# Optimization experiments

Hardware: AMD Instinct MI355X
Metric: run time of the kernel (lower is better)

## Reference

```python
import jax, jax.numpy as jnp
import numpy as np


def setup_inputs() -> dict:
    key = jax.random.key(0)
    ks = jax.random.split(key, 9)
    B, T, C = 4, 2048, 2048
    E, I, SI = 8, 1408, 5632
    s = lambda k, shape, fan_in: jax.random.normal(k, shape, jnp.float32) * (fan_in ** -0.5)
    return {
        "x": jax.random.normal(ks[0], (B, T, C), jnp.float32),
        "gate_w": s(ks[1], (C, E), C),                  # router: x @ gate_w -> [N,E]
        "expert_gate_w": s(ks[2], (E, C, I), C),        # stacked gate_proj weights
        "expert_up_w": s(ks[3], (E, C, I), C),          # stacked up_proj weights
        "expert_down_w": s(ks[4], (E, I, C), I),        # stacked down_proj weights
        "shared_gate_w": s(ks[5], (C, SI), C),
        "shared_up_w": s(ks[6], (C, SI), C),
        "shared_down_w": s(ks[7], (SI, C), SI),
        "shared_expert_gate_w": s(ks[8], (C, 1), C),
        "top_k": 4,
    }


def reference(x, gate_w, expert_gate_w, expert_up_w, expert_down_w,
              shared_gate_w, shared_up_w, shared_down_w, shared_expert_gate_w, top_k):
    B, T, C = x.shape
    E = gate_w.shape[1]
    xf = x.reshape(-1, C)                      # [N, C]
    N = xf.shape[0]

    # --- router: softmax (fp32) -> top-k -> renormalize ---
    logits = xf @ gate_w                       # [N, E]
    probs = jax.nn.softmax(logits.astype(jnp.float32), axis=-1)
    w, idx = jax.lax.top_k(probs, top_k)       # [N, k]
    w = w / jnp.sum(w, axis=-1, keepdims=True)

    # dense combine gates [N, E]: zero for non-selected experts (equivalent to
    # the torch dispatch/sort/combine: each token gets weight w_k on expert idx_k)
    gates = jnp.zeros((N, E), jnp.float32).at[jnp.arange(N)[:, None], idx].add(w)

    # --- per-expert SwiGLU MLP, accumulated via scan over experts ---
    def step(acc, ew):
        wg, wu, wd, g = ew                     # wg/wu: [C,I], wd: [I,C], g: [N]
        h = jax.nn.silu(xf @ wg) * (xf @ wu)   # [N, I]
        return acc + g[:, None] * (h @ wd), None

    routed, _ = jax.lax.scan(
        step, jnp.zeros_like(xf),
        (expert_gate_w, expert_up_w, expert_down_w, gates.T))

    # --- shared expert with sigmoid gate ---
    shared = (jax.nn.silu(xf @ shared_gate_w) * (xf @ shared_up_w)) @ shared_down_w
    sg = jax.nn.sigmoid(xf @ shared_expert_gate_w)   # [N, 1]

    return (routed + sg * shared).reshape(B, T, C)
```

## Files before the change

### kernel.cpp

```cpp
#include <hip/hip_runtime.h>
#include <hip/hip_bf16.h>
#include <stdint.h>


typedef float f32x4 __attribute__((ext_vector_type(4)));
typedef int   i32x4 __attribute__((ext_vector_type(4)));
typedef __hip_bfloat16 bf16;

#define DEV __device__ __forceinline__

DEV void mfma16(f32x4& c, const i32x4& a, const i32x4& b) {
    asm("v_mfma_f32_16x16x32_bf16 %0, %1, %2, %0" : "+v"(c) : "v"(a), "v"(b));
}

template<int ROWS>
DEV void stage(const bf16* gtile, long ldK, char* lds, int tid) {
    const int wid = tid >> 6, lane = tid & 63;
    const int swz = ((lane & 7) ^ (lane >> 3)) << 4;
    constexpr int NISS = (ROWS * 128) / 4096;
    #pragma unroll
    for (int i = 0; i < NISS; i++) {
        const int o = i * 4096 + wid * 1024;
        const int row = (o >> 7) + (lane >> 3);
        const char* ga = (const char*)gtile + (long)row * (ldK * 2) + swz;
        __builtin_amdgcn_global_load_lds(
            (const __attribute__((address_space(1))) void*)ga,
            (__attribute__((address_space(3))) void*)(lds + o), 16, 0, 0);
    }
}

template<int ROWS>
DEV void stage_idx(const char* base, const long* roff, int ktb, char* lds,
                   int tid, int swz) {
    const int wid = tid >> 6;
    constexpr int NISS = (ROWS * 128) / 4096;
    #pragma unroll
    for (int i = 0; i < NISS; i++) {
        const int o = i * 4096 + wid * 1024;
        const char* ga = base + roff[i] + ktb + swz;
        __builtin_amdgcn_global_load_lds(
            (const __attribute__((address_space(1))) void*)ga,
            (__attribute__((address_space(3))) void*)(lds + o), 16, 0, 0);
    }
}

DEV i32x4 ldsfrag(const char* lds, int row, int kbyte) {
    const int off = (row << 7) + (kbyte ^ ((row & 7) << 4));
    return *(const i32x4*)(lds + off);
}

__global__ __launch_bounds__(256) void tcvt(const float* __restrict__ srcA,
        bf16* __restrict__ dstA, const float* __restrict__ srcB,
        bf16* __restrict__ dstB, int Cd, long dld, long sz, long dz,
        int zsplit) {
    __shared__ float t[64][65];
    long z = blockIdx.z;
    const float* src; bf16* dst;
    if ((int)z < zsplit) { src = srcA; dst = dstA; }
    else { src = srcB; dst = dstB; z -= zsplit; }
    src += z * sz; dst += z * dz;
    const int cb = blockIdx.x * 64, rb = blockIdx.y * 64;
    const int tx = threadIdx.x & 63, ty = threadIdx.x >> 6;
    #pragma unroll
    for (int i = 0; i < 16; i++) {
        const int r = ty + i * 4;
        t[r][tx] = src[(long)(rb + r) * Cd + cb + tx];
    }
    __syncthreads();
    #pragma unroll
    for (int i = 0; i < 16; i++) {
        const int c = ty + i * 4;
        dst[(long)(cb + c) * dld + rb + tx] = __float2bfloat16(t[tx][c]);
    }
}

__global__ __launch_bounds__(256) void cvtrt(const float* __restrict__ x,
        const float* __restrict__ gw, const float* __restrict__ segw,
        bf16* __restrict__ xb, int* __restrict__ tidx, float* __restrict__ tw,
        float* __restrict__ sg) {
    const int lane = threadIdx.x & 63;
    const long t = (long)blockIdx.x * 4 + (threadIdx.x >> 6);
    const float4* xr = (const float4*)(x + t * 2048);
    ushort4* xo = (ushort4*)(xb + t * 2048);
    float a[9];
    #pragma unroll
    for (int e = 0; e < 9; e++) a[e] = 0.f;
    #pragma unroll
    for (int i = 0; i < 8; i++) {
        const int c4 = i * 64 + lane;
        const float4 v = xr[c4];
        union { bf16 h[4]; ushort4 u; } cu;
        cu.h[0] = __float2bfloat16(v.x); cu.h[1] = __float2bfloat16(v.y);
        cu.h[2] = __float2bfloat16(v.z); cu.h[3] = __float2bfloat16(v.w);
        xo[c4] = cu.u;
        const int c = c4 * 4;
        const float xv[4] = { v.x, v.y, v.z, v.w };
        #pragma unroll
        for (int j = 0; j < 4; j++) {
            const float4* g4 = (const float4*)(gw + (long)(c + j) * 8);
            const float4 g0 = g4[0], g1 = g4[1];
            a[0] += xv[j] * g0.x; a[1] += xv[j] * g0.y;
            a[2] += xv[j] * g0.z; a[3] += xv[j] * g0.w;
            a[4] += xv[j] * g1.x; a[5] += xv[j] * g1.y;
            a[6] += xv[j] * g1.z; a[7] += xv[j] * g1.w;
            a[8] += xv[j] * segw[c + j];
        }
    }
    #pragma unroll
    for (int e = 0; e < 9; e++) {
        #pragma unroll
        for (int o = 32; o; o >>= 1) a[e] += __shfl_xor(a[e], o, 64);
    }
    if (lane == 0) {
        float m = a[0];
        #pragma unroll
        for (int e = 1; e < 8; e++) m = fmaxf(m, a[e]);
        float p[8]; float s = 0.f;
        #pragma unroll
        for (int e = 0; e < 8; e++) { p[e] = expf(a[e] - m); s += p[e]; }
        #pragma unroll
        for (int e = 0; e < 8; e++) p[e] /= s;
        bool used[8] = {false,false,false,false,false,false,false,false};
        float wsum = 0.f; int idx[4]; float wv[4];
        for (int k = 0; k < 4; k++) {
            float best = -1.f; int bi = 0;
            for (int e = 0; e < 8; e++)
                if (!used[e] && p[e] > best) { best = p[e]; bi = e; }
            used[bi] = true; idx[k] = bi; wv[k] = best; wsum += best;
        }
        int4 iv; float4 wv4;
        iv.x = idx[0]; iv.y = idx[1]; iv.z = idx[2]; iv.w = idx[3];
        wv4.x = wv[0] / wsum; wv4.y = wv[1] / wsum;
        wv4.z = wv[2] / wsum; wv4.w = wv[3] / wsum;
        ((int4*)tidx)[t] = iv;
        ((float4*)tw)[t] = wv4;
        sg[t] = 1.f / (1.f + expf(-a[8]));
    }
}

__global__ __launch_bounds__(256) void build_lists(const int* __restrict__ tidx,
        const float* __restrict__ tw, int* __restrict__ tok,
        float* __restrict__ wl, int* __restrict__ cnt, int N) {
    const int e = blockIdx.x;
    const int tid = threadIdx.x;
    const int per = N / 256;
    __shared__ int csum[256];
    int c = 0;
    for (int i = 0; i < per; i++) {
        const int4 id4 = ((const int4*)tidx)[tid * per + i];
        if (id4.x == e || id4.y == e || id4.z == e || id4.w == e) c++;
    }
    csum[tid] = c;
    __syncthreads();
    for (int o = 1; o < 256; o <<= 1) {
        const int v = (tid >= o) ? csum[tid - o] : 0;
        __syncthreads();
        csum[tid] += v;
        __syncthreads();
    }
    int pos = csum[tid] - c;
    if (tid == 255) cnt[e] = csum[255];
    for (int i = 0; i < per; i++) {
        const int t = tid * per + i;
        const int4   id4 = ((const int4*)tidx)[t];
        const float4 w4  = ((const float4*)tw)[t];
        float w = 0.f; int hit = 0;
        if      (id4.x == e) { w = w4.x; hit = 1; }
        else if (id4.y == e) { w = w4.y; hit = 1; }
        else if (id4.z == e) { w = w4.z; hit = 1; }
        else if (id4.w == e) { w = w4.w; hit = 1; }
        if (hit) { tok[(long)e * N + pos] = t; wl[(long)e * N + pos] = w; pos++; }
    }
}

__global__ void scan8(const int* __restrict__ cnt, int* __restrict__ starts) {
    if (threadIdx.x == 0) {
        int s = 0;
        for (int e = 0; e < 8; e++) { starts[e] = s; s += cnt[e]; }
        starts[8] = s;
    }
}

__global__ __launch_bounds__(256) void megadual(const bf16* __restrict__ A0,
        const int* __restrict__ tok, const int* __restrict__ cnt,
        const int* __restrict__ starts, int nExpZ, int e0,
        const bf16* __restrict__ Wea, const bf16* __restrict__ Web, long ebz,
        const bf16* __restrict__ Wsa, const bf16* __restrict__ Wsb,
        bf16* __restrict__ He, bf16* __restrict__ Hs,
        const float* __restrict__ wl, const float* __restrict__ sg, int K) {
    __shared__ __align__(128) char Al[16384];
    __shared__ __align__(128) char Gl[8192];
    __shared__ __align__(128) char Ul[8192];
    const int z = blockIdx.z;
    const bf16 *BG, *BU; bf16* H; long hld, n0; const float* sc;
    const int* ridx; int Me;
    if (z < nExpZ) {
        const int e = e0 + z;
        Me = cnt[e];
        ridx = tok + (long)e * 8192;
        BG = Wea + (long)z * ebz; BU = Web + (long)z * ebz;
        H = He + ((long)starts[e] - starts[e0]) * 1408;
        hld = 1408; sc = wl + (long)e * 8192;
        n0 = (long)blockIdx.y * 64;
    } else {
        Me = 8192; ridx = nullptr;
        BG = Wsa; BU = Wsb; H = Hs; hld = 5632; sc = sg;
        n0 = (long)((z - nExpZ) * gridDim.y + blockIdx.y) * 64;
    }
    const long m0 = (long)blockIdx.x * 128;
    if (m0 >= Me) return;
    const int tid = threadIdx.x, lane = tid & 63, wid = tid >> 6;
    const int wm = (wid >> 1) * 64, wn = (wid & 1) * 32;
    const int l15 = lane & 15, lhi = lane >> 4;
    const int swz = ((lane & 7) ^ (lane >> 3)) << 4;
    long roffA[4];
    #pragma unroll
    for (int i = 0; i < 4; i++) {
        const int rit = ((i * 4096 + wid * 1024) >> 7) + (lane >> 3);
        int g = (int)m0 + rit;
        if (ridx) g = ridx[g < Me ? g : Me - 1];
        roffA[i] = (long)g * (K * 2);
    }
    f32x4 ag[4][2] = {}; f32x4 au[4][2] = {};
    for (int kt = 0; kt < K; kt += 64) {
        stage_idx<128>((const char*)A0, roffA, kt * 2, Al, tid, swz);
        stage<64>(BG + n0 * K + kt, (long)K, Gl, tid);
        stage<64>(BU + n0 * K + kt, (long)K, Ul, tid);
        __syncthreads();
        #pragma unroll
        for (int ks = 0; ks < 2; ks++) {
            const int kb = ks * 64 + lhi * 16;
            i32x4 af[4], bg[2], bu[2];
            #pragma unroll
            for (int mi = 0; mi < 4; mi++) af[mi] = ldsfrag(Al, wm + mi * 16 + l15, kb);
            #pragma unroll
            for (int ni = 0; ni < 2; ni++) {
                bg[ni] = ldsfrag(Gl, wn + ni * 16 + l15, kb);
                bu[ni] = ldsfrag(Ul, wn + ni * 16 + l15, kb);
            }
            #pragma unroll
            for (int mi = 0; mi < 4; mi++) {
                #pragma unroll
                for (int ni = 0; ni < 2; ni++) {
                    mfma16(ag[mi][ni], af[mi], bg[ni]);
                    mfma16(au[mi][ni], af[mi], bu[ni]);
                }
            }
        }
        __syncthreads();
    }
    asm volatile("s_nop 7\n\ts_nop 7\n\ts_nop 7");
    #pragma unroll
    for (int mi = 0; mi < 4; mi++) {
        #pragma unroll
        for (int r = 0; r < 4; r++) {
            const int pos = (int)m0 + wm + mi * 16 + lhi * 4 + r;
            if (pos < Me) {
                const float s = sc[pos];
                #pragma unroll
                for (int ni = 0; ni < 2; ni++) {
                    const float gv = ag[mi][ni][r], uv = au[mi][ni][r];
                    const float h = (gv / (1.f + expf(-gv))) * uv * s;
                    H[(long)pos * hld + n0 + wn + ni * 16 + l15] = __float2bfloat16(h);
                }
            }
        }
    }
}

template<int TAG>
__global__ __launch_bounds__(256) void gemm_down_t(const bf16* __restrict__ A,
        const bf16* __restrict__ BT, float* __restrict__ C,
        const int* __restrict__ ridx, const int* __restrict__ cntp, int Mfix,
        const int* __restrict__ starts, int ia, int ib,
        int K, long ldc, int beta) {
    __shared__ __align__(128) char Al[16384];
    __shared__ __align__(128) char Bl[16384];
    const int Me = cntp ? *cntp : Mfix;
    const long m0 = (long)blockIdx.y * 128;
    if (m0 >= Me) return;
    if (starts) A += ((long)starts[ia] - starts[ib]) * K;
    const int tid = threadIdx.x, lane = tid & 63, wid = tid >> 6;
    const long n0 = (long)blockIdx.x * 128;
    const int wm = (wid >> 1) * 64, wn = (wid & 1) * 64;
    const int l15 = lane & 15, lhi = lane >> 4;
    f32x4 acc[4][4] = {};
    for (int kt = 0; kt < K; kt += 64) {
        stage<128>(A  + m0 * K + kt, (long)K, Al, tid);
        stage<128>(BT + n0 * K + kt, (long)K, Bl, tid);
        __syncthreads();
        #pragma unroll
        for (int ks = 0; ks < 2; ks++) {
            const int kb = ks * 64 + lhi * 16;
            i32x4 af[4], bfr[4];
            #pragma unroll
            for (int mi = 0; mi < 4; mi++) af[mi]  = ldsfrag(Al, wm + mi * 16 + l15, kb);
            #pragma unroll
            for (int ni = 0; ni < 4; ni++) bfr[ni] = ldsfrag(Bl, wn + ni * 16 + l15, kb);
            #pragma unroll
            for (int mi = 0; mi < 4; mi++) {
                #pragma unroll
                for (int ni = 0; ni < 4; ni++) mfma16(acc[mi][ni], af[mi], bfr[ni]);
            }
        }
        __syncthreads();
    }
    asm volatile("s_nop 7\n\ts_nop 7\n\ts_nop 7");
    #pragma unroll
    for (int mi = 0; mi < 4; mi++) {
        #pragma unroll
        for (int r = 0; r < 4; r++) {
            const int pos = (int)m0 + wm + mi * 16 + lhi * 4 + r;
            if (pos < Me) {
                const long orow = ridx ? (long)ridx[pos] : (long)pos;
                #pragma unroll
                for (int ni = 0; ni < 4; ni++) {
                    const long ci = orow * ldc + n0 + wn + ni * 16 + l15;
                    float v = acc[mi][ni][r];
                    if (beta) v += C[ci];
                    C[ci] = v;
                }
            }
        }
    }
}

extern "C" void kernel_launch(void* const* d_in, const int* in_sizes, int n_in,
                              void* d_out, int out_size, void* d_ws, size_t ws_size,
                              hipStream_t stream) {
    const int N = 8192, Cdim = 2048, E = 8, I = 1408, SI = 5632;

    const float* x    = (const float*)d_in[0];
    const float* gw   = (const float*)d_in[1];
    const float* egw  = (const float*)d_in[2];
    const float* euw  = (const float*)d_in[3];
    const float* edw  = (const float*)d_in[4];
    const float* sgw  = (const float*)d_in[5];
    const float* suw  = (const float*)d_in[6];
    const float* sdw  = (const float*)d_in[7];
    const float* segw = (const float*)d_in[8];
    float* out = (float*)d_out;

    char* ws = (char*)d_ws;
    size_t off = 0;
    auto alloc = [&](size_t bytes) { char* p = ws + off; off += (bytes + 255) & ~(size_t)255; return p; };

    bf16*  xb     = (bf16*) alloc((size_t)N * Cdim * 2);
    int*   tidx   = (int*)  alloc((size_t)N * 4 * 4);
    float* tw     = (float*)alloc((size_t)N * 4 * 4);
    float* sg     = (float*)alloc((size_t)N * 4);
    int*   tok    = (int*)  alloc((size_t)E * N * 4);
    float* wl     = (float*)alloc((size_t)E * N * 4);
    int*   cnt    = (int*)  alloc(256);
    int*   starts = (int*)  alloc(256);
    const size_t commonEnd = off;

    const size_t EWSLOT = (size_t)E * I * Cdim * 2;
    const size_t SWSLOT = (size_t)SI * Cdim * 2;
    const size_t HROWS  = (size_t)4 * N;
    const size_t mergedNeed = commonEnd + 2 * EWSLOT + 2 * SWSLOT
                            + (size_t)N * SI * 2 + HROWS * I * 2 + 4096;

    cvtrt<<<N / 4, 256, 0, stream>>>(x, gw, segw, xb, tidx, tw, sg);
    build_lists<<<E, 256, 0, stream>>>(tidx, tw, tok, wl, cnt, N);
    scan8<<<1, 64, 0, stream>>>(cnt, starts);

    if (ws_size >= mergedNeed) {
        bf16* Wea = (bf16*)alloc(EWSLOT);
        bf16* Web = (bf16*)alloc(EWSLOT);
        bf16* Wsa = (bf16*)alloc(SWSLOT);
        bf16* Wsb = (bf16*)alloc(SWSLOT);
        bf16* Hs  = (bf16*)alloc((size_t)N * SI * 2);
        bf16* He  = (bf16*)alloc(HROWS * I * 2);
        bf16* Wsc = Wea;
        bf16* Wec = Web;

        tcvt<<<dim3(SI / 64, Cdim / 64, 2), 256, 0, stream>>>(
                sgw, Wsa, suw, Wsb, SI, (long)Cdim, 0, 0, 1);
        tcvt<<<dim3(I / 64, Cdim / 64, 2 * E), 256, 0, stream>>>(
                egw, Wea, euw, Web, I, (long)Cdim,
                (long)Cdim * I, (long)I * Cdim, E);

        megadual<<<dim3(N / 128, I / 64, E + 4), 256, 0, stream>>>(xb,
                tok, cnt, starts, E, 0, Wea, Web, (long)I * Cdim,
                Wsa, Wsb, He, Hs, wl, sg, Cdim);

        tcvt<<<dim3(Cdim / 64, SI / 64, 1), 256, 0, stream>>>(
                sdw, Wsc, nullptr, nullptr, Cdim, (long)SI, 0, 0, 1);
        tcvt<<<dim3(Cdim / 64, I / 64, E), 256, 0, stream>>>(
                edw, Wec, nullptr, nullptr, Cdim, (long)I,
                (long)I * Cdim, (long)Cdim * I, E);

        gemm_down_t<0><<<dim3(Cdim / 128, N / 128), 256, 0, stream>>>(
                Hs, Wsc, out, nullptr, nullptr, N, nullptr, 0, 0,
                SI, (long)Cdim, 0);
        for (int e = 0; e < E; e++) {
            gemm_down_t<1><<<dim3(Cdim / 128, N / 128), 256, 0, stream>>>(
                    He, Wec + (long)e * Cdim * I, out,
                    tok + (long)e * N, cnt + e, 0, starts, e, 0,
                    I, (long)Cdim, 1);
        }
        return;
    }

    bf16* Wa = (bf16*)alloc(SWSLOT);
    bf16* Wb = (bf16*)alloc(SWSLOT);
    bf16* Wc = (bf16*)alloc(SWSLOT);
    bf16* Hs = (bf16*)alloc((size_t)N * SI * 2);
    bf16* He = (bf16*)alloc(HROWS * I * 2);
    if (off > ws_size) return;

    tcvt<<<dim3(SI / 64, Cdim / 64, 2), 256, 0, stream>>>(
            sgw, Wa, suw, Wb, SI, (long)Cdim, 0, 0, 1);
    tcvt<<<dim3(Cdim / 64, SI / 64, 1), 256, 0, stream>>>(
            sdw, Wc, nullptr, nullptr, Cdim, (long)SI, 0, 0, 1);
    megadual<<<dim3(N / 128, I / 64, 4), 256, 0, stream>>>(xb,
            tok, cnt, starts, 0, 0, nullptr, nullptr, 0,
            Wa, Wb, nullptr, Hs, wl, sg, Cdim);
    gemm_down_t<0><<<dim3(Cdim / 128, N / 128), 256, 0, stream>>>(
            Hs, Wc, out, nullptr, nullptr, N, nullptr, 0, 0, SI, (long)Cdim, 0);

    for (int b = 0; b < 2; b++) {
        const int e0 = b * 4;
        tcvt<<<dim3(I / 64, Cdim / 64, 8), 256, 0, stream>>>(
                egw + (long)e0 * Cdim * I, Wa, euw + (long)e0 * Cdim * I, Wb,
                I, (long)Cdim, (long)Cdim * I, (long)I * Cdim, 4);
        megadual<<<dim3(N / 128, I / 64, 4), 256, 0, stream>>>(xb,
                tok, cnt, starts, 4, e0, Wa, Wb, (long)I * Cdim,
                nullptr, nullptr, He, nullptr, wl, sg, Cdim);
        tcvt<<<dim3(Cdim / 64, I / 64, 4), 256, 0, stream>>>(
                edw + (long)e0 * I * Cdim, Wc, nullptr, nullptr,
                Cdim, (long)I, (long)I * Cdim, (long)Cdim * I, 4);
        for (int z = 0; z < 4; z++) {
            gemm_down_t<1><<<dim3(Cdim / 128, N / 128), 256, 0, stream>>>(
                    He, Wc + (long)z * Cdim * I, out,
                    tok + (long)(e0 + z) * N, cnt + e0 + z, 0,
                    starts, e0 + z, e0, I, (long)Cdim, 1);
        }
    }
}
```

Measured before the change: 1.576 ms.

## Batch expert down-projections into one grouped GEMM and reduce per token

The eight per-expert down-projection launches, each doing a read-modify-write scatter into the fp32 output, are replaced by a single grouped GEMM over all experts. It writes bf16 per-slot results into a contiguous buffer, and a reduce kernel sums each token's four slots into the output. build_lists now records an inverse map from token and k to list position. Workspace regions for the converted down weights and intermediates are reused. This trades fewer launches and less serialized fp32 traffic for an extra bf16 intermediate round-trip and some bf16 rounding of the expert outputs. The combine weight is still not applied in the down GEMM, so it is presumably folded into He earlier.

```diff
diff --git a/kernel.cpp b/kernel.cpp
--- a/kernel.cpp
+++ b/kernel.cpp
@@ -140,7 +140,8 @@
 
 __global__ __launch_bounds__(256) void build_lists(const int* __restrict__ tidx,
         const float* __restrict__ tw, int* __restrict__ tok,
-        float* __restrict__ wl, int* __restrict__ cnt, int N) {
+        float* __restrict__ wl, int* __restrict__ cnt, int* __restrict__ inv,
+        int N) {
     const int e = blockIdx.x;
     const int tid = threadIdx.x;
     const int per = N / 256;
@@ -164,12 +165,17 @@
         const int t = tid * per + i;
         const int4   id4 = ((const int4*)tidx)[t];
         const float4 w4  = ((const float4*)tw)[t];
-        float w = 0.f; int hit = 0;
-        if      (id4.x == e) { w = w4.x; hit = 1; }
-        else if (id4.y == e) { w = w4.y; hit = 1; }
-        else if (id4.z == e) { w = w4.z; hit = 1; }
-        else if (id4.w == e) { w = w4.w; hit = 1; }
-        if (hit) { tok[(long)e * N + pos] = t; wl[(long)e * N + pos] = w; pos++; }
+        float w = 0.f; int hit = 0; int k = 0;
+        if      (id4.x == e) { w = w4.x; hit = 1; k = 0; }
+        else if (id4.y == e) { w = w4.y; hit = 1; k = 1; }
+        else if (id4.z == e) { w = w4.z; hit = 1; k = 2; }
+        else if (id4.w == e) { w = w4.w; hit = 1; k = 3; }
+        if (hit) {
+            tok[(long)e * N + pos] = t;
+            wl[(long)e * N + pos] = w;
+            inv[t * 4 + k] = pos;
+            pos++;
+        }
     }
 }
 
@@ -325,6 +331,90 @@
     }
 }
 
+__global__ __launch_bounds__(256) void megadown(const bf16* __restrict__ He,
+        const bf16* __restrict__ Wd0, long wz, bf16* __restrict__ De,
+        const int* __restrict__ cnt, const int* __restrict__ starts, int K) {
+    __shared__ __align__(128) char Al[16384];
+    __shared__ __align__(128) char Bl[16384];
+    const int z = blockIdx.z;
+    const int Me = cnt[z];
+    const long m0 = (long)blockIdx.y * 128;
+    if (m0 >= Me) return;
+    const bf16* A  = He + (long)starts[z] * K;
+    const bf16* BT = Wd0 + (long)z * wz;
+    const int tid = threadIdx.x, lane = tid & 63, wid = tid >> 6;
+    const long n0 = (long)blockIdx.x * 128;
+    const int wm = (wid >> 1) * 64, wn = (wid & 1) * 64;
+    const int l15 = lane & 15, lhi = lane >> 4;
+    f32x4 acc[4][4] = {};
+    for (int kt = 0; kt < K; kt += 64) {
+        stage<128>(A  + m0 * K + kt, (long)K, Al, tid);
+        stage<128>(BT + n0 * K + kt, (long)K, Bl, tid);
+        __syncthreads();
+        #pragma unroll
+        for (int ks = 0; ks < 2; ks++) {
+            const int kb = ks * 64 + lhi * 16;
+            i32x4 af[4], bfr[4];
+            #pragma unroll
+            for (int mi = 0; mi < 4; mi++) af[mi]  = ldsfrag(Al, wm + mi * 16 + l15, kb);
+            #pragma unroll
+            for (int ni = 0; ni < 4; ni++) bfr[ni] = ldsfrag(Bl, wn + ni * 16 + l15, kb);
+            #pragma unroll
+            for (int mi = 0; mi < 4; mi++) {
+                #pragma unroll
+                for (int ni = 0; ni < 4; ni++) mfma16(acc[mi][ni], af[mi], bfr[ni]);
+            }
+        }
+        __syncthreads();
+    }
+    asm volatile("s_nop 7\n\ts_nop 7\n\ts_nop 7");
+    #pragma unroll
+    for (int mi = 0; mi < 4; mi++) {
+        #pragma unroll
+        for (int r = 0; r < 4; r++) {
+            const int pos = (int)m0 + wm + mi * 16 + lhi * 4 + r;
+            if (pos < Me) {
+                const long orow = (long)starts[z] + pos;
+                #pragma unroll
+                for (int ni = 0; ni < 4; ni++) {
+                    De[orow * 2048 + n0 + wn + ni * 16 + l15]
+                        = __float2bfloat16(acc[mi][ni][r]);
+                }
+            }
+        }
+    }
+}
+
+__global__ __launch_bounds__(256) void reduce4(const bf16* __restrict__ De,
+        const int* __restrict__ tidx, const int* __restrict__ inv,
+        const int* __restrict__ starts, float* __restrict__ out) {
+    const long t = blockIdx.x;
+    const int c = threadIdx.x * 8;
+    const int4 e4 = ((const int4*)tidx)[t];
+    const int4 p4 = ((const int4*)inv)[t];
+    long r[4];
+    r[0] = (long)starts[e4.x] + p4.x; r[1] = (long)starts[e4.y] + p4.y;
+    r[2] = (long)starts[e4.z] + p4.z; r[3] = (long)starts[e4.w] + p4.w;
+    float4* o = (float4*)(out + t * 2048 + c);
+    float4 o0 = o[0], o1 = o[1];
+    float acc[8] = { o0.x, o0.y, o0.z, o0.w, o1.x, o1.y, o1.z, o1.w };
+    #pragma unroll
+    for (int k = 0; k < 4; k++) {
+        const uint4 v = *(const uint4*)(De + r[k] * 2048 + c);
+        const unsigned w[4] = { v.x, v.y, v.z, v.w };
+        #pragma unroll
+        for (int j = 0; j < 4; j++) {
+            union { unsigned u; float f; } lo, hi;
+            lo.u = (w[j] & 0xffffu) << 16;
+            hi.u = w[j] & 0xffff0000u;
+            acc[j * 2]     += lo.f;
+            acc[j * 2 + 1] += hi.f;
+        }
+    }
+    o[0] = make_float4(acc[0], acc[1], acc[2], acc[3]);
+    o[1] = make_float4(acc[4], acc[5], acc[6], acc[7]);
+}
+
 extern "C" void kernel_launch(void* const* d_in, const int* in_sizes, int n_in,
                               void* d_out, int out_size, void* d_ws, size_t ws_size,
                               hipStream_t stream) {
@@ -351,6 +441,7 @@
     float* sg     = (float*)alloc((size_t)N * 4);
     int*   tok    = (int*)  alloc((size_t)E * N * 4);
     float* wl     = (float*)alloc((size_t)E * N * 4);
+    int*   inv    = (int*)  alloc((size_t)N * 4 * 4);
     int*   cnt    = (int*)  alloc(256);
     int*   starts = (int*)  alloc(256);
     const size_t commonEnd = off;
@@ -362,18 +453,20 @@
                             + (size_t)N * SI * 2 + HROWS * I * 2 + 4096;
 
     cvtrt<<<N / 4, 256, 0, stream>>>(x, gw, segw, xb, tidx, tw, sg);
-    build_lists<<<E, 256, 0, stream>>>(tidx, tw, tok, wl, cnt, N);
+    build_lists<<<E, 256, 0, stream>>>(tidx, tw, tok, wl, cnt, inv, N);
     scan8<<<1, 64, 0, stream>>>(cnt, starts);
 
     if (ws_size >= mergedNeed) {
-        bf16* Wea = (bf16*)alloc(EWSLOT);
-        bf16* Web = (bf16*)alloc(EWSLOT);
-        bf16* Wsa = (bf16*)alloc(SWSLOT);
-        bf16* Wsb = (bf16*)alloc(SWSLOT);
+        char* wreg = (char*)alloc(2 * EWSLOT + 2 * SWSLOT);
+        bf16* Wea = (bf16*)wreg;
+        bf16* Web = (bf16*)(wreg + EWSLOT);
+        bf16* Wsa = (bf16*)(wreg + 2 * EWSLOT);
+        bf16* Wsb = (bf16*)(wreg + 2 * EWSLOT + SWSLOT);
         bf16* Hs  = (bf16*)alloc((size_t)N * SI * 2);
         bf16* He  = (bf16*)alloc(HROWS * I * 2);
-        bf16* Wsc = Wea;
-        bf16* Wec = Web;
+        bf16* Wsd = xb;
+        bf16* Wed = Hs;
+        bf16* De  = (bf16*)wreg;
 
         tcvt<<<dim3(SI / 64, Cdim / 64, 2), 256, 0, stream>>>(
                 sgw, Wsa, suw, Wsb, SI, (long)Cdim, 0, 0, 1);
@@ -386,20 +479,17 @@
                 Wsa, Wsb, He, Hs, wl, sg, Cdim);
 
         tcvt<<<dim3(Cdim / 64, SI / 64, 1), 256, 0, stream>>>(
-                sdw, Wsc, nullptr, nullptr, Cdim, (long)SI, 0, 0, 1);
+                sdw, Wsd, nullptr, nullptr, Cdim, (long)SI, 0, 0, 1);
+        gemm_down_t<0><<<dim3(Cdim / 128, N / 128), 256, 0, stream>>>(
+                Hs, Wsd, out, nullptr, nullptr, N, nullptr, 0, 0,
+                SI, (long)Cdim, 0);
+
         tcvt<<<dim3(Cdim / 64, I / 64, E), 256, 0, stream>>>(
-                edw, Wec, nullptr, nullptr, Cdim, (long)I,
+                edw, Wed, nullptr, nullptr, Cdim, (long)I,
                 (long)I * Cdim, (long)Cdim * I, E);
-
-        gemm_down_t<0><<<dim3(Cdim / 128, N / 128), 256, 0, stream>>>(
-                Hs, Wsc, out, nullptr, nullptr, N, nullptr, 0, 0,
-                SI, (long)Cdim, 0);
-        for (int e = 0; e < E; e++) {
-            gemm_down_t<1><<<dim3(Cdim / 128, N / 128), 256, 0, stream>>>(
-                    He, Wec + (long)e * Cdim * I, out,
-                    tok + (long)e * N, cnt + e, 0, starts, e, 0,
-                    I, (long)Cdim, 1);
-        }
+        megadown<<<dim3(Cdim / 128, N / 128, E), 256, 0, stream>>>(
+                He, Wed, (long)Cdim * I, De, cnt, starts, I);
+        reduce4<<<N, 256, 0, stream>>>(De, tidx, inv, starts, out);
         return;
     }
 
```

New measurement: 1.382 ms (median of 2 runs). 12.3% less time.
